# Kernel optimization log

Hardware: AMD Instinct MI355X
Metric: run time of the kernel (lower is better)

Reference implementation:

```python
import jax, jax.numpy as jnp
import numpy as np

C, H_IMG = 1, 1024
N_PATCH = 64
L = 12          # blocks
NH = 12         # heads
D = 768         # hidden_d
DH = D // NH    # head dim
MLP = 4 * D
OUT_D = 1000
BATCH = 256
PATCH = H_IMG // N_PATCH
IN_D = C * PATCH
SEQ = N_PATCH + 1


def _pos_emb(pos, dim):
    # faithful to original: exponent uses i directly (2*i/dim), sin for even i, cos for odd i
    p = np.arange(pos, dtype=np.float64)[:, None]
    i = np.arange(dim, dtype=np.float64)[None, :]
    ang = p / np.power(10000.0, 2.0 * i / dim)
    pe = np.where((np.arange(dim)[None, :] % 2) == 0, np.sin(ang), np.cos(ang))
    return jnp.asarray(pe, dtype=jnp.float32)


def setup_inputs() -> dict:
    key = jax.random.key(0)
    ks = jax.random.split(key, 24)
    s = lambda fan: 1.0 / np.sqrt(fan)
    inp = {
        "images": jax.random.normal(ks[0], (BATCH, C, H_IMG), jnp.float32),
        "linear_w": jax.random.uniform(ks[1], (D, IN_D), jnp.float32, -s(IN_D), s(IN_D)),
        "linear_b": jax.random.uniform(ks[2], (D,), jnp.float32, -s(IN_D), s(IN_D)),
        "class_token": jax.random.uniform(ks[3], (1, D), jnp.float32),
        "pos_emb": _pos_emb(SEQ, D),
        "ln1_g": jnp.ones((L, D), jnp.float32),
        "ln1_b": jnp.zeros((L, D), jnp.float32),
        "wq": jax.random.uniform(ks[4], (L, NH, DH, DH), jnp.float32, -s(DH), s(DH)),
        "bq": jax.random.uniform(ks[5], (L, NH, DH), jnp.float32, -s(DH), s(DH)),
        "wk": jax.random.uniform(ks[6], (L, NH, DH, DH), jnp.float32, -s(DH), s(DH)),
        "bk": jax.random.uniform(ks[7], (L, NH, DH), jnp.float32, -s(DH), s(DH)),
        "wv": jax.random.uniform(ks[8], (L, NH, DH, DH), jnp.float32, -s(DH), s(DH)),
        "bv": jax.random.uniform(ks[9], (L, NH, DH), jnp.float32, -s(DH), s(DH)),
        "ln2_g": jnp.ones((L, D), jnp.float32),
        "ln2_b": jnp.zeros((L, D), jnp.float32),
        "w1": jax.random.uniform(ks[10], (L, MLP, D), jnp.float32, -s(D), s(D)),
        "b1": jax.random.uniform(ks[11], (L, MLP), jnp.float32, -s(D), s(D)),
        "w2": jax.random.uniform(ks[12], (L, D, MLP), jnp.float32, -s(MLP), s(MLP)),
        "b2": jax.random.uniform(ks[13], (L, D), jnp.float32, -s(MLP), s(MLP)),
        "head_w": jax.random.uniform(ks[14], (OUT_D, D), jnp.float32, -s(D), s(D)),
        "head_b": jax.random.uniform(ks[15], (OUT_D,), jnp.float32, -s(D), s(D)),
    }
    return inp


def _ln(x, g, b):
    m = jnp.mean(x, axis=-1, keepdims=True)
    v = jnp.var(x, axis=-1, keepdims=True)
    return (x - m) / jnp.sqrt(v + 1e-5) * g + b


def _block(x, g1, be1, wq, bq, wk, bk, wv, bv, g2, be2, w1, bb1, w2, bb2):
    B, S, _ = x.shape
    h = _ln(x, g1, be1).reshape(B, S, NH, DH)  # split heads along feature dim
    q = jnp.einsum('bshd,hed->bshe', h, wq) + bq
    k = jnp.einsum('bshd,hed->bshe', h, wk) + bk
    v = jnp.einsum('bshd,hed->bshe', h, wv) + bv
    scores = jnp.einsum('bshe,bthe->bhst', q, k) / np.sqrt(DH).astype(np.float32)
    attn = jax.nn.softmax(scores, axis=-1)
    o = jnp.einsum('bhst,bthe->bshe', attn, v).reshape(B, S, D)
    x = x + o
    h2 = _ln(x, g2, be2)
    m = jax.nn.gelu(jnp.einsum('bsd,fd->bsf', h2, w1) + bb1, approximate=False)
    m = jnp.einsum('bsf,df->bsd', m, w2) + bb2
    return x + m


def reference(images, linear_w, linear_b, class_token, pos_emb,
              ln1_g, ln1_b, wq, bq, wk, bk, wv, bv, ln2_g, ln2_b,
              w1, b1, w2, b2, head_w, head_b):
    n = images.shape[0]
    # patchify: [n, c, h] -> [n, n_patch, c*patch_size] (flatten is (c, patch) row-major)
    patches = images.reshape(n, C, N_PATCH, PATCH).transpose(0, 2, 1, 3).reshape(n, N_PATCH, IN_D)
    tokens = jnp.einsum('npi,di->npd', patches, linear_w) + linear_b
    cls = jnp.broadcast_to(class_token[None], (n, 1, D))
    x = jnp.concatenate([cls, tokens], axis=1) + pos_emb[None]
    for l in range(L):
        x = _block(x, ln1_g[l], ln1_b[l], wq[l], bq[l], wk[l], bk[l], wv[l], bv[l],
                   ln2_g[l], ln2_b[l], w1[l], b1[l], w2[l], b2[l])
    cls_out = x[:, 0]
    logits = cls_out @ head_w.T + head_b
    return jax.nn.softmax(logits, axis=-1)
```

## Files before the change

kernel.cpp:

```cpp
#include <hip/hip_runtime.h>

#define NLAYER 12
#define NHEAD  12
#define DHEAD  64
#define DMODEL 768
#define SEQL   65
#define NBATCH 256
#define MTOK   (NBATCH*SEQL)
#define MLPD   3072

typedef _Float16 f16;
typedef f16  f16x8 __attribute__((ext_vector_type(8)));
typedef f16  f16x4 __attribute__((ext_vector_type(4)));
typedef float f32x4 __attribute__((ext_vector_type(4)));

#define MFMA(a,b,c) __builtin_amdgcn_mfma_f32_16x16x32_f16(a,b,c,0,0,0)

__device__ __forceinline__ void gload16(const void* g, void* l) {
  __builtin_amdgcn_global_load_lds((const __attribute__((address_space(1))) void*)g,
                                   (__attribute__((address_space(3))) void*)l, 16, 0, 0);
}

__device__ __forceinline__ float gelu_f(float v) {
  float z = fabsf(v) * 0.70710678118654752f;
  float t = 1.f / (1.f + 0.3275911f * z);
  float p = ((((1.061405429f*t - 1.453152027f)*t + 1.421413741f)*t
              - 0.284496736f)*t + 0.254829592f)*t;
  float erfz = 1.f - p * __expf(-z*z);
  float erfv = copysignf(erfz, v);
  return 0.5f * v * (1.f + erfv);
}

__global__ __launch_bounds__(256) void cvt_f16k(const float* __restrict__ in,
                                                f16* __restrict__ out, int n) {
  long i = ((long)blockIdx.x*256 + threadIdx.x)*4;
  if (i >= n) return;
  const float4 v = *(const float4*)(in + i);
  f16x4 o = { (f16)v.x, (f16)v.y, (f16)v.z, (f16)v.w };
  *(f16x4*)(out + i) = o;
}

__global__ __launch_bounds__(256) void patch_embed(
    const float* __restrict__ images, const float* __restrict__ lw,
    const float* __restrict__ lb, const float* __restrict__ cls,
    const float* __restrict__ pe, float* __restrict__ x) {
  const int s = blockIdx.x, n = blockIdx.y, tid = threadIdx.x;
  __shared__ float p[16];
  if (s > 0 && tid < 16) p[tid] = images[(long)n*1024 + (s-1)*16 + tid];
  __syncthreads();
  float* xr = x + ((long)n*SEQL + s)*DMODEL;
  #pragma unroll
  for (int j = 0; j < 3; ++j) {
    int d = tid + j*256;
    float v;
    if (s == 0) {
      v = cls[d] + pe[d];
    } else {
      float acc = lb[d];
      #pragma unroll
      for (int i = 0; i < 16; ++i) acc += p[i]*lw[d*16+i];
      v = acc + pe[s*DMODEL + d];
    }
    xr[d] = v;
  }
}

__global__ __launch_bounds__(256) void ln_kernel(
    const float* __restrict__ x, const float* __restrict__ g,
    const float* __restrict__ b, f16* __restrict__ out) {
  const int row = blockIdx.x, tid = threadIdx.x;
  const float* xr = x + (long)row*DMODEL;
  float v0 = xr[tid], v1 = xr[tid+256], v2 = xr[tid+512];
  float s = v0+v1+v2;
  float s2 = v0*v0 + v1*v1 + v2*v2;
  #pragma unroll
  for (int o = 32; o >= 1; o >>= 1) { s += __shfl_xor(s, o); s2 += __shfl_xor(s2, o); }
  __shared__ float red[8];
  const int wave = tid>>6, lane = tid&63;
  if (lane == 0) { red[wave] = s; red[4+wave] = s2; }
  __syncthreads();
  s  = red[0]+red[1]+red[2]+red[3];
  s2 = red[4]+red[5]+red[6]+red[7];
  float mean = s * (1.f/768.f);
  float var  = s2 * (1.f/768.f) - mean*mean;
  float rstd = rsqrtf(var + 1e-5f);
  f16* orow = out + (long)row*DMODEL;
  orow[tid]     = (f16)((v0-mean)*rstd*g[tid]     + b[tid]);
  orow[tid+256] = (f16)((v1-mean)*rstd*g[tid+256] + b[tid+256]);
  orow[tid+512] = (f16)((v2-mean)*rstd*g[tid+512] + b[tid+512]);
}

__global__ __launch_bounds__(256) void attn_kernel(
    const f16* __restrict__ h, const f16* __restrict__ wq, const f16* __restrict__ wk,
    const f16* __restrict__ wv, const float* __restrict__ bq, const float* __restrict__ bk,
    const float* __restrict__ bv, float* __restrict__ x) {
  __shared__ __align__(16) f16 HsPs[80*104];
  __shared__ __align__(16) f16 Qs[80*72];
  __shared__ __align__(16) f16 Ks[80*72];
  __shared__ __align__(16) f16 Vt[64*104];
  const int hd = blockIdx.x, b = blockIdx.y;
  const int tid = threadIdx.x, wave = tid>>6, lane = tid&63;
  const int lc = lane & 15, lg = lane >> 4;
  const f16* hbase = h + ((long)b*SEQL)*DMODEL + hd*DHEAD;

  for (int c = tid; c < 80*8; c += 256) {
    int s = c >> 3, ec = (c & 7)*8;
    uint4 val = {0u,0u,0u,0u};
    if (s < SEQL) val = *(const uint4*)(hbase + (long)s*DMODEL + ec);
    *(uint4*)&HsPs[s*104 + ec] = val;
  }
  for (int c = tid; c < 64*104/8; c += 256) {
    uint4 z = {0u,0u,0u,0u};
    *(uint4*)&Vt[c*8] = z;
  }
  __syncthreads();

  for (int task = wave; task < 15; task += 4) {
    int mat = task / 5, mt = task % 5;
    const f16* W = (mat == 0 ? wq : mat == 1 ? wk : wv) + hd*DHEAD*DHEAD;
    const float* bias = (mat == 0 ? bq : mat == 1 ? bk : bv) + hd*DHEAD;
    #pragma unroll
    for (int nt = 0; nt < 4; ++nt) {
      f32x4 a = {0.f,0.f,0.f,0.f};
      #pragma unroll
      for (int kt = 0; kt < 2; ++kt) {
        f16x8 af = *(const f16x8*)&HsPs[(mt*16 + lc)*104 + kt*32 + lg*8];
        f16x8 bf = *(const f16x8*)&W[(nt*16 + lc)*DHEAD + kt*32 + lg*8];
        a = MFMA(af, bf, a);
      }
      float bb = bias[nt*16 + lc];
      #pragma unroll
      for (int r = 0; r < 4; ++r) {
        int s = mt*16 + lg*4 + r;
        int e = nt*16 + lc;
        float v = a[r] + bb;
        if (mat == 0)      Qs[s*72 + e] = (f16)v;
        else if (mat == 1) Ks[s*72 + e] = (f16)v;
        else               Vt[e*104 + s] = (f16)v;
      }
    }
  }
  __syncthreads();

  for (int mt = wave; mt < 5; mt += 4) {
    {
      uint2 z = {0u,0u};
      *(uint2*)&HsPs[(mt*16 + (lane>>2))*104 + 80 + (lane&3)*4] = z;
    }
    f32x4 sc[5];
    #pragma unroll
    for (int nt = 0; nt < 5; ++nt) {
      f32x4 a = {0.f,0.f,0.f,0.f};
      #pragma unroll
      for (int kt = 0; kt < 2; ++kt) {
        f16x8 af = *(const f16x8*)&Qs[(mt*16 + lc)*72 + kt*32 + lg*8];
        f16x8 bf = *(const f16x8*)&Ks[(nt*16 + lc)*72 + kt*32 + lg*8];
        a = MFMA(af, bf, a);
      }
      sc[nt] = a;
    }
    #pragma unroll
    for (int r = 0; r < 4; ++r) {
      float vals[5];
      #pragma unroll
      for (int nt = 0; nt < 5; ++nt) {
        float v = sc[nt][r]*0.125f;
        if (nt*16 + lc > 64) v = -1e30f;
        vals[nt] = v;
      }
      float mx = vals[0];
      #pragma unroll
      for (int nt = 1; nt < 5; ++nt) mx = fmaxf(mx, vals[nt]);
      #pragma unroll
      for (int o = 8; o >= 1; o >>= 1) mx = fmaxf(mx, __shfl_xor(mx, o, 16));
      float sum = 0.f, p[5];
      #pragma unroll
      for (int nt = 0; nt < 5; ++nt) { p[nt] = __expf(vals[nt]-mx); sum += p[nt]; }
      #pragma unroll
      for (int o = 8; o >= 1; o >>= 1) sum += __shfl_xor(sum, o, 16);
      float inv = 1.f/sum;
      int row = mt*16 + lg*4 + r;
      #pragma unroll
      for (int nt = 0; nt < 5; ++nt) HsPs[row*104 + nt*16 + lc] = (f16)(p[nt]*inv);
    }
    f32x4 oacc[4];
    #pragma unroll
    for (int nt = 0; nt < 4; ++nt) {
      f32x4 a = {0.f,0.f,0.f,0.f};
      #pragma unroll
      for (int kt = 0; kt < 3; ++kt) {
        f16x8 af = *(const f16x8*)&HsPs[(mt*16 + lc)*104 + kt*32 + lg*8];
        f16x8 bf = *(const f16x8*)&Vt[(nt*16 + lc)*104 + kt*32 + lg*8];
        a = MFMA(af, bf, a);
      }
      oacc[nt] = a;
    }
    float* xb = x + ((long)b*SEQL)*DMODEL + hd*DHEAD;
    #pragma unroll
    for (int nt = 0; nt < 4; ++nt) {
      #pragma unroll
      for (int r = 0; r < 4; ++r) {
        int s = mt*16 + lg*4 + r;
        if (s < SEQL) {
          int e = nt*16 + lc;
          xb[(long)s*DMODEL + e] += oacc[nt][r];
        }
      }
    }
  }
}

template<int ACT>
__global__ __launch_bounds__(256, 3) void gemm128(
    const f16* __restrict__ A, const f16* __restrict__ B,
    const float* __restrict__ bias, void* __restrict__ Cout,
    int M, int N, int K) {
  __shared__ __align__(16) f16 lds[24576];
  const int tid = threadIdx.x;
  const int wave = tid >> 6, lane = tid & 63;
  const int lrow = lane & 15, lk = lane >> 4;
  const int wm = (wave >> 1) * 64, wn = (wave & 1) * 64;

  const int gx = gridDim.x;
  const int nwg = gx * gridDim.y;
  const int orig = blockIdx.y * gx + blockIdx.x;
  const int q = nwg >> 3, r = nwg & 7;
  const int xcd = orig & 7, lin = orig >> 3;
  const int wgid = (xcd < r ? xcd*(q+1) : r*(q+1) + (xcd - r)*q) + lin;
  const int bx = wgid % gx, by = wgid / gx;

  const long m0 = (long)by * 128, n0 = (long)bx * 128;

  f32x4 acc[4][4];
  #pragma unroll
  for (int i = 0; i < 4; ++i)
    #pragma unroll
    for (int j = 0; j < 4; ++j) acc[i][j] = (f32x4){0.f,0.f,0.f,0.f};

  const int NT = K >> 5;
  auto stage = [&](int t) {
    const int s = t % 3;
    f16* As = &lds[s*4096];
    f16* Bs = &lds[12288 + s*4096];
    #pragma unroll
    for (int i = 0; i < 2; ++i) {
      int c = tid + i*256;
      int row = c >> 2;
      int kp = (c & 3) ^ ((row >> 1) & 3);
      gload16(A + (m0 + row)*(long)K + t*32 + kp*8, &As[c*8]);
      gload16(B + (n0 + row)*(long)K + t*32 + kp*8, &Bs[c*8]);
    }
  };
  stage(0); stage(1);

  for (int t = 0; t < NT; ++t) {
    const int s = t % 3;
    const f16* As = &lds[s*4096];
    const f16* Bs = &lds[12288 + s*4096];
    if (t + 1 < NT) asm volatile("s_waitcnt vmcnt(4)" ::: "memory");
    else            asm volatile("s_waitcnt vmcnt(0)" ::: "memory");
    asm volatile("s_barrier" ::: "memory");
    if (t + 2 < NT) stage(t + 2);
    f16x8 af[4], bfr[4];
    #pragma unroll
    for (int mf = 0; mf < 4; ++mf) {
      int row = wm + mf*16 + lrow;
      af[mf] = *(const f16x8*)&As[row*32 + ((lk ^ ((row>>1)&3))*8)];
    }
    #pragma unroll
    for (int nf = 0; nf < 4; ++nf) {
      int row = wn + nf*16 + lrow;
      bfr[nf] = *(const f16x8*)&Bs[row*32 + ((lk ^ ((row>>1)&3))*8)];
    }
    __builtin_amdgcn_s_setprio(1);
    #pragma unroll
    for (int mf = 0; mf < 4; ++mf)
      #pragma unroll
      for (int nf = 0; nf < 4; ++nf)
        acc[mf][nf] = MFMA(af[mf], bfr[nf], acc[mf][nf]);
    __builtin_amdgcn_s_setprio(0);
  }

  __syncthreads();

  if (ACT == 0) {
    #pragma unroll
    for (int nf = 0; nf < 4; ++nf) {
      int col = wn + nf*16 + lrow;
      float bv = bias[(int)n0 + col];
      #pragma unroll
      for (int mf = 0; mf < 4; ++mf) {
        #pragma unroll
        for (int r2 = 0; r2 < 4; ++r2) {
          int row = wm + mf*16 + lk*4 + r2;
          float v = acc[mf][nf][r2] + bv;
          int byte = (row*256 + col*2) ^ (((row>>2)&7)<<4);
          *(f16*)((char*)lds + byte) = (f16)gelu_f(v);
        }
      }
    }
    __syncthreads();
    f16* Cf = (f16*)Cout;
    #pragma unroll
    for (int i = 0; i < 8; ++i) {
      int g = i*256 + tid;
      int row = g >> 4, ch = g & 15;
      int byte = (row*256 + ch*16) ^ (((row>>2)&7)<<4);
      f16x8 val = *(const f16x8*)((const char*)lds + byte);
      *(f16x8*)(Cf + (m0 + row)*(long)N + n0 + ch*8) = val;
    }
  } else {
    float* Cf = (float*)Cout;
    #pragma unroll
    for (int nf = 0; nf < 4; ++nf) {
      int col = (int)n0 + wn + nf*16 + lrow;
      float bv = bias[col];
      #pragma unroll
      for (int mf = 0; mf < 4; ++mf) {
        #pragma unroll
        for (int r2 = 0; r2 < 4; ++r2) {
          long row = m0 + wm + mf*16 + lk*4 + r2;
          Cf[row*(long)N + col] += acc[mf][nf][r2] + bv;
        }
      }
    }
  }
}

__global__ __launch_bounds__(256) void head_kernel(
    const float* __restrict__ x, const float* __restrict__ hw,
    const float* __restrict__ hb, float* __restrict__ out) {
  const int b = blockIdx.x, tid = threadIdx.x;
  __shared__ float cls[768];
  __shared__ float red[8];
  const float* xr = x + (long)b*SEQL*DMODEL;
  #pragma unroll
  for (int j = 0; j < 3; ++j) cls[tid + j*256] = xr[tid + j*256];
  __syncthreads();
  float lgv[4];
  #pragma unroll
  for (int j = 0; j < 4; ++j) {
    int c = tid + j*256;
    float acc = -1e30f;
    if (c < 1000) {
      const float* wr = hw + (long)c*768;
      float s_ = 0.f;
      for (int i = 0; i < 768; ++i) s_ += cls[i]*wr[i];
      acc = s_ + hb[c];
    }
    lgv[j] = acc;
  }
  const int wave = tid>>6, lane = tid&63;
  float mx = fmaxf(fmaxf(lgv[0],lgv[1]),fmaxf(lgv[2],lgv[3]));
  #pragma unroll
  for (int o = 32; o >= 1; o >>= 1) mx = fmaxf(mx, __shfl_xor(mx, o));
  if (lane == 0) red[wave] = mx;
  __syncthreads();
  mx = fmaxf(fmaxf(red[0],red[1]),fmaxf(red[2],red[3]));
  float e[4]; float sum = 0.f;
  #pragma unroll
  for (int j = 0; j < 4; ++j) {
    int c = tid + j*256;
    e[j] = (c < 1000) ? expf(lgv[j]-mx) : 0.f;
    sum += e[j];
  }
  #pragma unroll
  for (int o = 32; o >= 1; o >>= 1) sum += __shfl_xor(sum, o);
  if (lane == 0) red[4+wave] = sum;
  __syncthreads();
  sum = red[4]+red[5]+red[6]+red[7];
  float inv = 1.f/sum;
  #pragma unroll
  for (int j = 0; j < 4; ++j) {
    int c = tid + j*256;
    if (c < 1000) out[(long)b*1000 + c] = e[j]*inv;
  }
}

extern "C" void kernel_launch(void* const* d_in, const int* in_sizes, int n_in,
                              void* d_out, int out_size, void* d_ws, size_t ws_size,
                              hipStream_t stream) {
  const float* images     = (const float*)d_in[0];
  const float* linear_w   = (const float*)d_in[1];
  const float* linear_b   = (const float*)d_in[2];
  const float* class_tok  = (const float*)d_in[3];
  const float* pos_emb    = (const float*)d_in[4];
  const float* ln1_g      = (const float*)d_in[5];
  const float* ln1_b      = (const float*)d_in[6];
  const float* wq         = (const float*)d_in[7];
  const float* bq         = (const float*)d_in[8];
  const float* wk         = (const float*)d_in[9];
  const float* bk         = (const float*)d_in[10];
  const float* wv         = (const float*)d_in[11];
  const float* bv         = (const float*)d_in[12];
  const float* ln2_g      = (const float*)d_in[13];
  const float* ln2_b      = (const float*)d_in[14];
  const float* w1         = (const float*)d_in[15];
  const float* b1         = (const float*)d_in[16];
  const float* w2         = (const float*)d_in[17];
  const float* b2         = (const float*)d_in[18];
  const float* head_w     = (const float*)d_in[19];
  const float* head_b     = (const float*)d_in[20];

  char* ws = (char*)d_ws;
  float* xbuf = (float*)(ws + 0);
  f16*   hbuf = (f16*)(ws + 51118080);
  f16*   mbuf = (f16*)(ws + 76677120);
  f16*   w1all = (f16*)(ws + 178913280);
  f16*   w2all = (f16*)(ws + 235536384);
  f16*   wqbB  = (f16*)(ws + 292159488);
  f16*   wkbB  = (f16*)(ws + 293339136);
  f16*   wvbB  = (f16*)(ws + 294518784);
  f16*   w1b  = (f16*)(ws + 178913280);
  f16*   w2b  = (f16*)(ws + 183631872);
  f16*   wqbS = (f16*)(ws + 188350464);
  f16*   wkbS = (f16*)(ws + 189530112);
  f16*   wvbS = (f16*)(ws + 190709760);
  if (ws_size < 191889408ull) return;
  const bool big = ws_size >= 295698432ull;
  f16* wqb = big ? wqbB : wqbS;
  f16* wkb = big ? wkbB : wkbS;
  f16* wvb = big ? wvbB : wvbS;

  patch_embed<<<dim3(SEQL, NBATCH), 256, 0, stream>>>(images, linear_w, linear_b,
                                                      class_tok, pos_emb, xbuf);
  cvt_f16k<<<576, 256, 0, stream>>>(wq, wqb, 589824);
  cvt_f16k<<<576, 256, 0, stream>>>(wk, wkb, 589824);
  cvt_f16k<<<576, 256, 0, stream>>>(wv, wvb, 589824);
  if (big) {
    cvt_f16k<<<27648, 256, 0, stream>>>(w1, w1all, 28311552);
    cvt_f16k<<<27648, 256, 0, stream>>>(w2, w2all, 28311552);
  }

  for (int l = 0; l < NLAYER; ++l) {
    ln_kernel<<<MTOK, 256, 0, stream>>>(xbuf, ln1_g + l*768, ln1_b + l*768, hbuf);
    attn_kernel<<<dim3(NHEAD, NBATCH), 256, 0, stream>>>(
        hbuf, wqb + l*49152, wkb + l*49152, wvb + l*49152,
        bq + l*768, bk + l*768, bv + l*768, xbuf);
    ln_kernel<<<MTOK, 256, 0, stream>>>(xbuf, ln2_g + l*768, ln2_b + l*768, hbuf);
    f16* w1p = big ? (w1all + (long)l*2359296) : w1b;
    f16* w2p = big ? (w2all + (long)l*2359296) : w2b;
    if (!big) cvt_f16k<<<2304, 256, 0, stream>>>(w1 + (long)l*2359296, w1b, 2359296);
    gemm128<0><<<dim3(MLPD/128, MTOK/128), 256, 0, stream>>>(
        hbuf, w1p, b1 + l*3072, (void*)mbuf, MTOK, MLPD, DMODEL);
    if (!big) cvt_f16k<<<2304, 256, 0, stream>>>(w2 + (long)l*2359296, w2b, 2359296);
    gemm128<1><<<dim3(DMODEL/128, MTOK/128), 256, 0, stream>>>(
        mbuf, w2p, b2 + l*768, (void*)xbuf, MTOK, DMODEL, MLPD);
  }
  head_kernel<<<NBATCH, 256, 0, stream>>>(xbuf, head_w, head_b, (float*)d_out);
}
```

Baseline: 4.706 ms.

## Replace MLP GEMM with 256x128 tile, 512-thread, K64 split-prefetch pipeline

Swaps the 128x128, 256-thread MLP GEMM for a 256x128 tile run by 8 waves, with a K step of 64 and a 3-slot LDS ring. Each K step's prefetch is split into two halves, and each half is issued between the LDS fragment reads and the MFMA batches, so global loads overlap compute. The goal is more operand reuse per loaded byte and fewer pipeline barriers per unit of work. In exchange the kernel uses about 144KB of LDS, so only one workgroup fits per CU, and the grid is half as large.

Result: slower. 4.977 ms (+5.8%).

```diff
diff --git a/kernel.cpp b/kernel.cpp
--- a/kernel.cpp
+++ b/kernel.cpp
@@ -211,15 +211,15 @@
 }
 
 template<int ACT>
-__global__ __launch_bounds__(256, 3) void gemm128(
+__global__ __launch_bounds__(512, 2) void gemmP(
     const f16* __restrict__ A, const f16* __restrict__ B,
     const float* __restrict__ bias, void* __restrict__ Cout,
     int M, int N, int K) {
-  __shared__ __align__(16) f16 lds[24576];
+  __shared__ __align__(16) f16 lds[73728];
   const int tid = threadIdx.x;
-  const int wave = tid >> 6, lane = tid & 63;
-  const int lrow = lane & 15, lk = lane >> 4;
-  const int wm = (wave >> 1) * 64, wn = (wave & 1) * 64;
+  const int wid = tid >> 6, lane = tid & 63;
+  const int lrow = lane & 15, lg = lane >> 4;
+  const int wr = wid >> 1, wc = wid & 1;
 
   const int gx = gridDim.x;
   const int nwg = gx * gridDim.y;
@@ -229,7 +229,7 @@
   const int wgid = (xcd < r ? xcd*(q+1) : r*(q+1) + (xcd - r)*q) + lin;
   const int bx = wgid % gx, by = wgid / gx;
 
-  const long m0 = (long)by * 128, n0 = (long)bx * 128;
+  const long m0 = (long)by * 256, n0 = (long)bx * 128;
 
   f32x4 acc[4][4];
   #pragma unroll
@@ -237,65 +237,106 @@
     #pragma unroll
     for (int j = 0; j < 4; ++j) acc[i][j] = (f32x4){0.f,0.f,0.f,0.f};
 
-  const int NT = K >> 5;
-  auto stage = [&](int t) {
-    const int s = t % 3;
-    f16* As = &lds[s*4096];
-    f16* Bs = &lds[12288 + s*4096];
-    #pragma unroll
-    for (int i = 0; i < 2; ++i) {
-      int c = tid + i*256;
-      int row = c >> 2;
-      int kp = (c & 3) ^ ((row >> 1) & 3);
-      gload16(A + (m0 + row)*(long)K + t*32 + kp*8, &As[c*8]);
-      gload16(B + (n0 + row)*(long)K + t*32 + kp*8, &Bs[c*8]);
-    }
+  const int NT = K >> 6;
+  const int sr = tid >> 3, sc = tid & 7;
+  const long gRowOff = (long)sr * K + (sc ^ (sr & 7)) * 8;
+  const int dOff = sr*64 + sc*8;
+  const f16* Abase = A + m0 * K;
+  const f16* Bbase = B + n0 * K;
+
+  auto stage = [&](int slot, int t, int half) {
+    f16* Ab = &lds[slot * 16384];
+    f16* Bb = &lds[49152 + slot * 8192];
+    const f16* Ag = Abase + (long)half*128*K + t*64 + gRowOff;
+    gload16(Ag,              &Ab[half*8192 + dOff]);
+    gload16(Ag + (long)64*K, &Ab[half*8192 + 4096 + dOff]);
+    const f16* Bg = Bbase + (long)half*64*K + t*64 + gRowOff;
+    gload16(Bg, &Bb[half*4096 + dOff]);
   };
-  stage(0); stage(1);
-
+
+  stage(0, 0, 0); stage(0, 0, 1);
+  stage(1, 1, 0); stage(1, 1, 1);
+  asm volatile("s_waitcnt vmcnt(6)" ::: "memory");
+  asm volatile("s_barrier" ::: "memory");
+
+  const int rbA = (wr*64 + lrow)*64;
+  const int rbB = (wc*64 + lrow)*64;
+  const int x7 = lrow & 7;
+  const int cK0 = ((0 + lg) ^ x7) * 8;
+  const int cK1 = ((4 + lg) ^ x7) * 8;
+
+  int scur = 0, spre = 2;
   for (int t = 0; t < NT; ++t) {
-    const int s = t % 3;
-    const f16* As = &lds[s*4096];
-    const f16* Bs = &lds[12288 + s*4096];
-    if (t + 1 < NT) asm volatile("s_waitcnt vmcnt(4)" ::: "memory");
-    else            asm volatile("s_waitcnt vmcnt(0)" ::: "memory");
+    const f16* Ab = &lds[scur * 16384];
+    const f16* Bb = &lds[49152 + scur * 8192];
+    const bool pf = (t + 2) < NT;
+
+    f16x8 Bf[4][2], Af0[2][2];
+    #pragma unroll
+    for (int nf = 0; nf < 4; ++nf) {
+      Bf[nf][0] = *(const f16x8*)&Bb[rbB + nf*1024 + cK0];
+      Bf[nf][1] = *(const f16x8*)&Bb[rbB + nf*1024 + cK1];
+    }
+    #pragma unroll
+    for (int mf = 0; mf < 2; ++mf) {
+      Af0[mf][0] = *(const f16x8*)&Ab[rbA + mf*1024 + cK0];
+      Af0[mf][1] = *(const f16x8*)&Ab[rbA + mf*1024 + cK1];
+    }
+    if (pf) stage(spre, t+2, 0);
+    __builtin_amdgcn_s_setprio(1);
+    #pragma unroll
+    for (int mf = 0; mf < 2; ++mf)
+      #pragma unroll
+      for (int nf = 0; nf < 4; ++nf)
+        acc[mf][nf] = MFMA(Af0[mf][0], Bf[nf][0], acc[mf][nf]);
+    #pragma unroll
+    for (int mf = 0; mf < 2; ++mf)
+      #pragma unroll
+      for (int nf = 0; nf < 4; ++nf)
+        acc[mf][nf] = MFMA(Af0[mf][1], Bf[nf][1], acc[mf][nf]);
+    __builtin_amdgcn_s_setprio(0);
     asm volatile("s_barrier" ::: "memory");
-    if (t + 2 < NT) stage(t + 2);
-    f16x8 af[4], bfr[4];
-    #pragma unroll
-    for (int mf = 0; mf < 4; ++mf) {
-      int row = wm + mf*16 + lrow;
-      af[mf] = *(const f16x8*)&As[row*32 + ((lk ^ ((row>>1)&3))*8)];
-    }
+
+    f16x8 Af1[2][2];
+    #pragma unroll
+    for (int mf = 0; mf < 2; ++mf) {
+      Af1[mf][0] = *(const f16x8*)&Ab[rbA + (mf+2)*1024 + cK0];
+      Af1[mf][1] = *(const f16x8*)&Ab[rbA + (mf+2)*1024 + cK1];
+    }
+    if (pf) stage(spre, t+2, 1);
+    __builtin_amdgcn_s_setprio(1);
+    #pragma unroll
+    for (int mf = 0; mf < 2; ++mf)
+      #pragma unroll
+      for (int nf = 0; nf < 4; ++nf)
+        acc[2+mf][nf] = MFMA(Af1[mf][0], Bf[nf][0], acc[2+mf][nf]);
+    #pragma unroll
+    for (int mf = 0; mf < 2; ++mf)
+      #pragma unroll
+      for (int nf = 0; nf < 4; ++nf)
+        acc[2+mf][nf] = MFMA(Af1[mf][1], Bf[nf][1], acc[2+mf][nf]);
+    __builtin_amdgcn_s_setprio(0);
+    if (pf) asm volatile("s_waitcnt vmcnt(6)" ::: "memory");
+    else    asm volatile("s_waitcnt vmcnt(0)" ::: "memory");
+    asm volatile("s_barrier" ::: "memory");
+
+    scur = (scur == 2) ? 0 : scur + 1;
+    spre = (spre == 2) ? 0 : spre + 1;
+  }
+
+  if (ACT == 0) {
+    char* Ct = (char*)lds;
     #pragma unroll
     for (int nf = 0; nf < 4; ++nf) {
-      int row = wn + nf*16 + lrow;
-      bfr[nf] = *(const f16x8*)&Bs[row*32 + ((lk ^ ((row>>1)&3))*8)];
-    }
-    __builtin_amdgcn_s_setprio(1);
-    #pragma unroll
-    for (int mf = 0; mf < 4; ++mf)
-      #pragma unroll
-      for (int nf = 0; nf < 4; ++nf)
-        acc[mf][nf] = MFMA(af[mf], bfr[nf], acc[mf][nf]);
-    __builtin_amdgcn_s_setprio(0);
-  }
-
-  __syncthreads();
-
-  if (ACT == 0) {
-    #pragma unroll
-    for (int nf = 0; nf < 4; ++nf) {
-      int col = wn + nf*16 + lrow;
+      int col = wc*64 + nf*16 + lrow;
       float bv = bias[(int)n0 + col];
       #pragma unroll
       for (int mf = 0; mf < 4; ++mf) {
         #pragma unroll
         for (int r2 = 0; r2 < 4; ++r2) {
-          int row = wm + mf*16 + lk*4 + r2;
-          float v = acc[mf][nf][r2] + bv;
+          int row = wr*64 + mf*16 + lg*4 + r2;
           int byte = (row*256 + col*2) ^ (((row>>2)&7)<<4);
-          *(f16*)((char*)lds + byte) = (f16)gelu_f(v);
+          *(f16*)(Ct + byte) = (f16)gelu_f(acc[mf][nf][r2] + bv);
         }
       }
     }
@@ -303,23 +344,23 @@
     f16* Cf = (f16*)Cout;
     #pragma unroll
     for (int i = 0; i < 8; ++i) {
-      int g = i*256 + tid;
+      int g = i*512 + tid;
       int row = g >> 4, ch = g & 15;
-      int byte = (row*256 + ch*16) ^ (((row>>2)&7)<<4);
-      f16x8 val = *(const f16x8*)((const char*)lds + byte);
+      int byte = row*256 + (ch ^ ((row>>2)&7))*16;
+      f16x8 val = *(const f16x8*)(Ct + byte);
       *(f16x8*)(Cf + (m0 + row)*(long)N + n0 + ch*8) = val;
     }
   } else {
     float* Cf = (float*)Cout;
     #pragma unroll
     for (int nf = 0; nf < 4; ++nf) {
-      int col = (int)n0 + wn + nf*16 + lrow;
+      int col = (int)n0 + wc*64 + nf*16 + lrow;
       float bv = bias[col];
       #pragma unroll
       for (int mf = 0; mf < 4; ++mf) {
         #pragma unroll
         for (int r2 = 0; r2 < 4; ++r2) {
-          long row = m0 + wm + mf*16 + lk*4 + r2;
+          long row = m0 + wr*64 + mf*16 + lg*4 + r2;
           Cf[row*(long)N + col] += acc[mf][nf][r2] + bv;
         }
       }
@@ -441,10 +482,10 @@
     f16* w1p = big ? (w1all + (long)l*2359296) : w1b;
     f16* w2p = big ? (w2all + (long)l*2359296) : w2b;
     if (!big) cvt_f16k<<<2304, 256, 0, stream>>>(w1 + (long)l*2359296, w1b, 2359296);
-    gemm128<0><<<dim3(MLPD/128, MTOK/128), 256, 0, stream>>>(
+    gemmP<0><<<dim3(MLPD/128, MTOK/256), 512, 0, stream>>>(
         hbuf, w1p, b1 + l*3072, (void*)mbuf, MTOK, MLPD, DMODEL);
     if (!big) cvt_f16k<<<2304, 256, 0, stream>>>(w2 + (long)l*2359296, w2b, 2359296);
-    gemm128<1><<<dim3(DMODEL/128, MTOK/128), 256, 0, stream>>>(
+    gemmP<1><<<dim3(DMODEL/128, MTOK/256), 512, 0, stream>>>(
         mbuf, w2p, b2 + l*768, (void*)xbuf, MTOK, DMODEL, MLPD);
   }
   head_kernel<<<NBATCH, 256, 0, stream>>>(xbuf, head_w, head_b, (float*)d_out);
```
